# Kernel optimization log

Hardware: AMD Instinct MI355X
Metric: run time of the kernel (lower is better)

## Reference

```python
import jax, jax.numpy as jnp
import numpy as np

B, N, D, H = 8, 2048, 512, 512


def setup_inputs() -> dict:
    key = jax.random.key(0)
    kx, kwq, kbq, kwk, kbk = jax.random.split(key, 5)
    s = 1.0 / np.sqrt(D)
    return {
        "x": jax.random.normal(kx, (B, N, D), dtype=jnp.float32),
        "Wq": jax.random.uniform(kwq, (D, H), jnp.float32, -s, s),
        "bq": jax.random.uniform(kbq, (H,), jnp.float32, -s, s),
        "Wk": jax.random.uniform(kwk, (D, H), jnp.float32, -s, s),
        "bk": jax.random.uniform(kbk, (H,), jnp.float32, -s, s),
    }


def reference(x, Wq, bq, Wk, bk):
    # x: [B, N, D]
    q = jnp.einsum("bnd,dh->bnh", x, Wq) + bq          # [B, N, H]
    k = jnp.einsum("bnd,dh->bnh", x, Wk) + bk          # [B, N, H]
    energy = jnp.einsum("bih,bjh->bij", q, k)           # [B, N, N] (no scaling)
    # NOTE: softmax over dim=1 (the QUERY axis), not the usual key axis.
    attn = jax.nn.softmax(energy, axis=1)               # [B, N, N]
    out = jnp.einsum("bij,bjd->bid", attn, x)           # V = x
    return out
```

## Files before the change

### kernel.cpp

```cpp
#include <hip/hip_runtime.h>
#include <hip/hip_bf16.h>
#include <cstdio>

typedef float f32x4 __attribute__((ext_vector_type(4)));
typedef __bf16 bf16x8 __attribute__((ext_vector_type(8)));

static constexpr int Bn = 8, Nn = 2048, Dn = 512, Hn = 512;

__device__ __forceinline__ unsigned short f2bf(float x) {
    union { float f; unsigned int u; } v; v.f = x;
    unsigned int r = (v.u + 0x7FFFu + ((v.u >> 16) & 1u)) >> 16;
    return (unsigned short)r;
}
__device__ __forceinline__ float bf2f(unsigned short h) {
    union { unsigned int u; float f; } v; v.u = ((unsigned int)h) << 16;
    return v.f;
}

__device__ __forceinline__ void gload_lds16(const unsigned short* g, unsigned short* l) {
    __builtin_amdgcn_global_load_lds(
        (const __attribute__((address_space(1))) void*)g,
        (__attribute__((address_space(3))) void*)l,
        16, 0, 0);
}

__device__ __forceinline__ int xcd_swizzle(int lin, int nwg) {
    return (lin & 7) * (nwg >> 3) + (lin >> 3);
}

__global__ void cast_x_kernel(const float* __restrict__ x, unsigned short* __restrict__ xb, int n) {
    int i = (blockIdx.x * blockDim.x + threadIdx.x) * 8;
    if (i >= n) return;
    float4 a = *(const float4*)(x + i);
    float4 b = *(const float4*)(x + i + 4);
    unsigned short tmp[8] = {f2bf(a.x), f2bf(a.y), f2bf(a.z), f2bf(a.w),
                             f2bf(b.x), f2bf(b.y), f2bf(b.z), f2bf(b.w)};
    *(uint4*)(xb + i) = *(const uint4*)tmp;
}

__global__ __launch_bounds__(256) void transpose_cast_kernel(
    const float* __restrict__ in, unsigned short* __restrict__ out,
    const float* __restrict__ sdiv, int R, int C)
{
    __shared__ float tile[64][65];
    const int z = blockIdx.z;
    const float* inb = in + (size_t)z * R * C;
    unsigned short* outb = out + (size_t)z * R * C;
    const int r0 = blockIdx.y * 64, c0 = blockIdx.x * 64;
    const int tx = threadIdx.x & 63, ty = threadIdx.x >> 6;
#pragma unroll
    for (int p = 0; p < 64; p += 4) {
        const int r = p + ty;
        float v = inb[(size_t)(r0 + r) * C + c0 + tx];
        if (sdiv) v /= sdiv[(size_t)z * R + r0 + r];
        tile[r][tx] = v;
    }
    __syncthreads();
#pragma unroll
    for (int p = 0; p < 64; p += 4) {
        const int oc = p + ty;
        outb[(size_t)(c0 + oc) * R + r0 + tx] = f2bf(tile[tx][oc]);
    }
}

__global__ void combine_s_kernel(const float* __restrict__ s_part, float* __restrict__ s,
                                 int nblk, int total) {
    int i = blockIdx.x * blockDim.x + threadIdx.x;
    if (i >= total) return;
    int z = i >> 11, j = i & (Nn - 1);
    float acc = 0.f;
    for (int p = 0; p < nblk; ++p) acc += s_part[((size_t)z * nblk + p) * Nn + j];
    s[i] = acc;
}

template<int MODE>
__global__ __launch_bounds__(512, 2) void gemm8p(
    const unsigned short* __restrict__ A, long long sA, int lda,
    const unsigned short* __restrict__ Bt, long long sB, int ldb,
    void* __restrict__ Cp, long long sC,
    const float* __restrict__ bias, const float* __restrict__ bias2, int bsplit,
    float* __restrict__ s_part,
    int M, int N, int K, int gx, int gy)
{
    __shared__ unsigned short As[4][8192];
    __shared__ unsigned short Bs[4][8192];

    const int lin = xcd_swizzle(blockIdx.x, gridDim.x);
    const int bz = lin / (gx * gy);
    const int rem = lin - bz * gx * gy;
    const int by = rem / gx;
    const int bx = rem - by * gx;

    const unsigned short* Ab = A + (size_t)bz * sA;
    const unsigned short* Bb = Bt + (size_t)bz * sB;
    const int i0 = by * 256, j0 = bx * 256;

    const int t = threadIdx.x;
    const int lane = t & 63;
    const int w = t >> 6;
    const int wm = w >> 2, wn = w & 3;
    const int l15 = lane & 15, g = lane >> 4;

    const int rd_off = (l15 * 4 + (g ^ ((l15 >> 1) & 3))) * 16;
    const int grow = lane >> 2;
    const int gk = ((lane & 3) ^ ((lane >> 3) & 3)) * 8;

    f32x4 acc[8][4];
    const f32x4 zero4 = {0.f, 0.f, 0.f, 0.f};
#pragma unroll
    for (int mi = 0; mi < 8; ++mi)
#pragma unroll
        for (int nf = 0; nf < 4; ++nf) acc[mi][nf] = zero4;

    const int NT = K >> 6;

#define STAGE(baseP, ldP, r0P, ldsP, Tn, kh)                                             \
    {                                                                                    \
        const int _slot = ((Tn) & 1) * 2 + (kh);                                         \
        const unsigned short* _src = (baseP) + (size_t)((r0P) + w * 16 + grow) * (ldP)   \
                                     + (Tn) * 64 + (kh) * 32 + gk;                       \
        gload_lds16(_src, &ldsP[_slot][w * 512]);                                        \
        gload_lds16(_src + (size_t)128 * (ldP), &ldsP[_slot][(w + 8) * 512]);            \
    }

    STAGE(Ab, lda, i0, As, 0, 0);
    STAGE(Bb, ldb, j0, Bs, 0, 0);
    STAGE(Ab, lda, i0, As, 0, 1);
    STAGE(Bb, ldb, j0, Bs, 0, 1);

    bf16x8 bfv[4];

    for (int T = 0; T < NT; ++T) {
        const int sbase = (T & 1) * 2;
        const bool last = (T == NT - 1);
#pragma unroll
        for (int q = 0; q < 4; ++q) {
            const int kk = q >> 1, mh = q & 1;
            if (q == 0) {
                asm volatile("s_waitcnt vmcnt(4)" ::: "memory");
                asm volatile("s_barrier" ::: "memory");
            } else if (q == 2) {
                if (last) asm volatile("s_waitcnt vmcnt(0)" ::: "memory");
                else      asm volatile("s_waitcnt vmcnt(4)" ::: "memory");
                asm volatile("s_barrier" ::: "memory");
            }
            const char* Bbase = (const char*)&Bs[sbase + kk][0] + (wn * 4) * 1024 + rd_off;
            if (mh == 0) {
#pragma unroll
                for (int nf = 0; nf < 4; ++nf)
                    bfv[nf] = *(const bf16x8*)(Bbase + nf * 1024);
            }
            const char* Abase = (const char*)&As[sbase + kk][0] + (wm * 8 + mh * 4) * 1024 + rd_off;
            bf16x8 af[4];
#pragma unroll
            for (int mf = 0; mf < 4; ++mf)
                af[mf] = *(const bf16x8*)(Abase + mf * 1024);
            if (!last) {
                if (q == 0)      STAGE(Ab, lda, i0, As, T + 1, 0)
                else if (q == 1) STAGE(Bb, ldb, j0, Bs, T + 1, 0)
                else if (q == 2) STAGE(Ab, lda, i0, As, T + 1, 1)
                else             STAGE(Bb, ldb, j0, Bs, T + 1, 1)
            }
            __builtin_amdgcn_s_setprio(1);
#pragma unroll
            for (int mf = 0; mf < 4; ++mf)
#pragma unroll
                for (int nf = 0; nf < 4; ++nf)
                    acc[mh * 4 + mf][nf] =
                        __builtin_amdgcn_mfma_f32_16x16x32_bf16(af[mf], bfv[nf], acc[mh * 4 + mf][nf], 0, 0, 0);
            __builtin_amdgcn_s_setprio(0);
            asm volatile("s_barrier" ::: "memory");
        }
    }
#undef STAGE

    if (MODE == 0) {
        unsigned short* C = (unsigned short*)Cp;
#pragma unroll
        for (int nf = 0; nf < 4; ++nf) {
            const int col = j0 + wn * 64 + nf * 16 + l15;
            const float bv = (col < bsplit) ? bias[col] : bias2[col - bsplit];
#pragma unroll
            for (int mi = 0; mi < 8; ++mi) {
                const int rb = i0 + wm * 128 + (mi >> 2) * 64 + (mi & 3) * 16 + g * 4;
#pragma unroll
                for (int r = 0; r < 4; ++r)
                    C[(size_t)(rb + r) * N + col] = f2bf(acc[mi][nf][r] + bv);
            }
        }
    } else {
        unsigned short* C = (unsigned short*)Cp + (size_t)bz * sC;
        float cs[4] = {0.f, 0.f, 0.f, 0.f};
#pragma unroll
        for (int nf = 0; nf < 4; ++nf) {
            const int col = j0 + wn * 64 + nf * 16 + l15;
#pragma unroll
            for (int mi = 0; mi < 8; ++mi) {
                const int rb = i0 + wm * 128 + (mi >> 2) * 64 + (mi & 3) * 16 + g * 4;
#pragma unroll
                for (int r = 0; r < 4; ++r) {
                    const float e = __expf(acc[mi][nf][r]);
                    const unsigned short h = f2bf(e);
                    C[(size_t)(rb + r) * N + col] = h;
                    cs[nf] += bf2f(h);
                }
            }
        }
#pragma unroll
        for (int nf = 0; nf < 4; ++nf) {
            cs[nf] += __shfl_xor(cs[nf], 16);
            cs[nf] += __shfl_xor(cs[nf], 32);
        }
        __syncthreads();
        float* red = (float*)&As[0][0];
        if (g == 0) {
#pragma unroll
            for (int nf = 0; nf < 4; ++nf)
                red[wm * 256 + wn * 64 + nf * 16 + l15] = cs[nf];
        }
        __syncthreads();
        if (t < 256)
            s_part[((size_t)bz * gy + by) * Nn + j0 + t] = red[t] + red[256 + t];
    }
}

template<int MODE>
__global__ __launch_bounds__(256, 2) void gemm_bt(
    const unsigned short* __restrict__ A, long long sA, int lda,
    const unsigned short* __restrict__ Bt, long long sB, int ldb,
    void* __restrict__ Cp, long long sC,
    int M, int N, int K, int gx, int gy)
{
    __shared__ unsigned short As[128 * 64];
    __shared__ unsigned short Bs[128 * 64];

    const int lin = xcd_swizzle(blockIdx.x, gridDim.x);
    const int bz = lin / (gx * gy);
    const int rem = lin - bz * gx * gy;
    const int by = rem / gx;
    const int bx = rem - by * gx;

    const unsigned short* Ab = A + (size_t)bz * sA;
    const unsigned short* Bb = Bt + (size_t)bz * sB;
    const int i0 = by * 128, j0 = bx * 128;

    const int t = threadIdx.x;
    const int lane = t & 63;
    const int wave = t >> 6;
    const int wr = wave >> 1, wc = wave & 1;
    const int l15 = lane & 15, g = lane >> 4;

    f32x4 acc[4][4];
    const f32x4 zero4 = {0.f, 0.f, 0.f, 0.f};
#pragma unroll
    for (int mi = 0; mi < 4; ++mi)
#pragma unroll
        for (int ni = 0; ni < 4; ++ni) acc[mi][ni] = zero4;

    const int rbase = wave * 32;
    const int lrow = lane >> 3;
    const int gch = (lane & 7) ^ lrow;

    for (int kt = 0; kt < K; kt += 64) {
#pragma unroll
        for (int i = 0; i < 4; ++i) {
            const int r = rbase + i * 8 + lrow;
            gload_lds16(Ab + (size_t)(i0 + r) * lda + kt + gch * 8, As + (rbase + i * 8) * 64);
            gload_lds16(Bb + (size_t)(j0 + r) * ldb + kt + gch * 8, Bs + (rbase + i * 8) * 64);
        }
        __syncthreads();
#pragma unroll
        for (int kk = 0; kk < 64; kk += 32) {
            const int sl0 = (kk >> 3) + g;
            bf16x8 af[4], bfr[4];
#pragma unroll
            for (int mi = 0; mi < 4; ++mi) {
                const int row = wr * 64 + mi * 16 + l15;
                af[mi] = *(const bf16x8*)(As + row * 64 + ((sl0 ^ (row & 7)) * 8));
            }
#pragma unroll
            for (int ni = 0; ni < 4; ++ni) {
                const int row = wc * 64 + ni * 16 + l15;
                bfr[ni] = *(const bf16x8*)(Bs + row * 64 + ((sl0 ^ (row & 7)) * 8));
            }
#pragma unroll
            for (int mi = 0; mi < 4; ++mi)
#pragma unroll
                for (int ni = 0; ni < 4; ++ni)
                    acc[mi][ni] = __builtin_amdgcn_mfma_f32_16x16x32_bf16(af[mi], bfr[ni], acc[mi][ni], 0, 0, 0);
        }
        __syncthreads();
    }

    float* C = (float*)Cp + (size_t)bz * sC;
#pragma unroll
    for (int ni = 0; ni < 4; ++ni) {
        const int col = j0 + wc * 64 + ni * 16 + l15;
#pragma unroll
        for (int mi = 0; mi < 4; ++mi) {
            const int rb = i0 + wr * 64 + mi * 16 + g * 4;
#pragma unroll
            for (int r = 0; r < 4; ++r)
                C[(size_t)(rb + r) * N + col] = acc[mi][ni][r];
        }
    }
}

extern "C" void kernel_launch(void* const* d_in, const int* in_sizes, int n_in,
                              void* d_out, int out_size, void* d_ws, size_t ws_size,
                              hipStream_t stream) {
    const float* x  = (const float*)d_in[0];
    const float* Wq = (const float*)d_in[1];
    const float* bq = (const float*)d_in[2];
    const float* Wk = (const float*)d_in[3];
    const float* bk = (const float*)d_in[4];
    float* out = (float*)d_out;

    char* ws = (char*)d_ws;
    unsigned short* xb    = (unsigned short*)(ws);
    unsigned short* qk    = (unsigned short*)(ws + (16ull << 20));
    unsigned short* WqkT  = (unsigned short*)(ws + (48ull << 20));
    unsigned short* xsT   = (unsigned short*)(ws + (49ull << 20));
    float*          s_prt = (float*)(ws + (65ull << 20));
    float*          s     = (float*)(ws + (66ull << 20));
    unsigned short* expE  = (unsigned short*)(ws + (67ull << 20));
    if (ws_size < (131ull << 20)) {
        fprintf(stderr, "WS TOO SMALL: have %zu need %llu\n", ws_size, (131ull << 20));
    }

    cast_x_kernel<<<dim3((Bn * Nn * Dn) / (8 * 256)), 256, 0, stream>>>(x, xb, Bn * Nn * Dn);
    transpose_cast_kernel<<<dim3(Hn / 64, Dn / 64, 1), 256, 0, stream>>>(Wq, WqkT, nullptr, Dn, Hn);
    transpose_cast_kernel<<<dim3(Hn / 64, Dn / 64, 1), 256, 0, stream>>>(Wk, WqkT + (size_t)Hn * Dn, nullptr, Dn, Hn);
    {
        const int gx = (2 * Hn) / 256, gy = (Bn * Nn) / 256;
        gemm8p<0><<<dim3(gx * gy), 512, 0, stream>>>(
            xb, 0, Dn, WqkT, 0, Dn, qk, 0, bq, bk, Hn, nullptr,
            Bn * Nn, 2 * Hn, Dn, gx, gy);
    }
    {
        const int gx = Nn / 256, gy = Nn / 256;
        gemm8p<1><<<dim3(gx * gy * Bn), 512, 0, stream>>>(
            qk, (long long)Nn * 2 * Hn, 2 * Hn,
            qk + Hn, (long long)Nn * 2 * Hn, 2 * Hn,
            expE, (long long)Nn * Nn, nullptr, nullptr, 0, s_prt,
            Nn, Nn, Hn, gx, gy);
    }
    combine_s_kernel<<<dim3((Bn * Nn) / 256), 256, 0, stream>>>(s_prt, s, Nn / 256, Bn * Nn);
    transpose_cast_kernel<<<dim3(Dn / 64, Nn / 64, Bn), 256, 0, stream>>>(x, xsT, s, Nn, Dn);
    {
        const int gx = Dn / 128, gy = Nn / 128;
        gemm_bt<2><<<dim3(gx * gy * Bn), 256, 0, stream>>>(
            expE, (long long)Nn * Nn, Nn, xsT, (long long)Dn * Nn, Nn,
            out, (long long)Nn * Dn, Nn, Dn, Nn, gx, gy);
    }
}
```

Measured before the change: 156.8 us.

## Double-buffer PV GEMM LDS and restructure gemm8p inner loop barriers

```diff
diff --git a/kernel.cpp b/kernel.cpp
--- a/kernel.cpp
+++ b/kernel.cpp
@@ -128,80 +128,110 @@
     STAGE(Ab, lda, i0, As, 0, 1);
     STAGE(Bb, ldb, j0, Bs, 0, 1);
 
-    bf16x8 bfv[4];
-
     for (int T = 0; T < NT; ++T) {
         const int sbase = (T & 1) * 2;
         const bool last = (T == NT - 1);
-#pragma unroll
-        for (int q = 0; q < 4; ++q) {
-            const int kk = q >> 1, mh = q & 1;
-            if (q == 0) {
-                asm volatile("s_waitcnt vmcnt(4)" ::: "memory");
-                asm volatile("s_barrier" ::: "memory");
-            } else if (q == 2) {
-                if (last) asm volatile("s_waitcnt vmcnt(0)" ::: "memory");
-                else      asm volatile("s_waitcnt vmcnt(4)" ::: "memory");
-                asm volatile("s_barrier" ::: "memory");
-            }
-            const char* Bbase = (const char*)&Bs[sbase + kk][0] + (wn * 4) * 1024 + rd_off;
-            if (mh == 0) {
+
+        asm volatile("s_waitcnt vmcnt(4)" ::: "memory");
+        asm volatile("s_barrier" ::: "memory");
+        {
+            const char* Bbase = (const char*)&Bs[sbase][0] + wn * 4096 + rd_off;
+            const char* Abase = (const char*)&As[sbase][0] + wm * 8192 + rd_off;
+            bf16x8 bfv[4], af[4];
+#pragma unroll
+            for (int nf = 0; nf < 4; ++nf) bfv[nf] = *(const bf16x8*)(Bbase + nf * 1024);
+#pragma unroll
+            for (int mf = 0; mf < 4; ++mf) af[mf] = *(const bf16x8*)(Abase + mf * 1024);
+            if (!last) STAGE(Ab, lda, i0, As, T + 1, 0);
+            __builtin_amdgcn_s_setprio(1);
+#pragma unroll
+            for (int mf = 0; mf < 4; ++mf)
 #pragma unroll
                 for (int nf = 0; nf < 4; ++nf)
-                    bfv[nf] = *(const bf16x8*)(Bbase + nf * 1024);
-            }
-            const char* Abase = (const char*)&As[sbase + kk][0] + (wm * 8 + mh * 4) * 1024 + rd_off;
-            bf16x8 af[4];
+                    acc[mf][nf] = __builtin_amdgcn_mfma_f32_16x16x32_bf16(af[mf], bfv[nf], acc[mf][nf], 0, 0, 0);
+            __builtin_amdgcn_s_setprio(0);
+            bf16x8 ag[4];
+#pragma unroll
+            for (int mf = 0; mf < 4; ++mf) ag[mf] = *(const bf16x8*)(Abase + 4096 + mf * 1024);
+            if (!last) STAGE(Bb, ldb, j0, Bs, T + 1, 0);
+            __builtin_amdgcn_s_setprio(1);
 #pragma unroll
             for (int mf = 0; mf < 4; ++mf)
-                af[mf] = *(const bf16x8*)(Abase + mf * 1024);
-            if (!last) {
-                if (q == 0)      STAGE(Ab, lda, i0, As, T + 1, 0)
-                else if (q == 1) STAGE(Bb, ldb, j0, Bs, T + 1, 0)
-                else if (q == 2) STAGE(Ab, lda, i0, As, T + 1, 1)
-                else             STAGE(Bb, ldb, j0, Bs, T + 1, 1)
-            }
+#pragma unroll
+                for (int nf = 0; nf < 4; ++nf)
+                    acc[4 + mf][nf] = __builtin_amdgcn_mfma_f32_16x16x32_bf16(ag[mf], bfv[nf], acc[4 + mf][nf], 0, 0, 0);
+            __builtin_amdgcn_s_setprio(0);
+        }
+
+        if (last) asm volatile("s_waitcnt vmcnt(0)" ::: "memory");
+        else      asm volatile("s_waitcnt vmcnt(4)" ::: "memory");
+        asm volatile("s_barrier" ::: "memory");
+        {
+            const char* Bbase = (const char*)&Bs[sbase + 1][0] + wn * 4096 + rd_off;
+            const char* Abase = (const char*)&As[sbase + 1][0] + wm * 8192 + rd_off;
+            bf16x8 bfv[4], af[4];
+#pragma unroll
+            for (int nf = 0; nf < 4; ++nf) bfv[nf] = *(const bf16x8*)(Bbase + nf * 1024);
+#pragma unroll
+            for (int mf = 0; mf < 4; ++mf) af[mf] = *(const bf16x8*)(Abase + mf * 1024);
+            if (!last) STAGE(Ab, lda, i0, As, T + 1, 1);
             __builtin_amdgcn_s_setprio(1);
 #pragma unroll
             for (int mf = 0; mf < 4; ++mf)
 #pragma unroll
                 for (int nf = 0; nf < 4; ++nf)
-                    acc[mh * 4 + mf][nf] =
-                        __builtin_amdgcn_mfma_f32_16x16x32_bf16(af[mf], bfv[nf], acc[mh * 4 + mf][nf], 0, 0, 0);
+                    acc[mf][nf] = __builtin_amdgcn_mfma_f32_16x16x32_bf16(af[mf], bfv[nf], acc[mf][nf], 0, 0, 0);
             __builtin_amdgcn_s_setprio(0);
-            asm volatile("s_barrier" ::: "memory");
+            bf16x8 ag[4];
+#pragma unroll
+            for (int mf = 0; mf < 4; ++mf) ag[mf] = *(const bf16x8*)(Abase + 4096 + mf * 1024);
+            if (!last) STAGE(Bb, ldb, j0, Bs, T + 1, 1);
+            __builtin_amdgcn_s_setprio(1);
+#pragma unroll
+            for (int mf = 0; mf < 4; ++mf)
+#pragma unroll
+                for (int nf = 0; nf < 4; ++nf)
+                    acc[4 + mf][nf] = __builtin_amdgcn_mfma_f32_16x16x32_bf16(ag[mf], bfv[nf], acc[4 + mf][nf], 0, 0, 0);
+            __builtin_amdgcn_s_setprio(0);
         }
     }
 #undef STAGE
 
     if (MODE == 0) {
         unsigned short* C = (unsigned short*)Cp;
+        float bv[4];
 #pragma unroll
         for (int nf = 0; nf < 4; ++nf) {
             const int col = j0 + wn * 64 + nf * 16 + l15;
-            const float bv = (col < bsplit) ? bias[col] : bias2[col - bsplit];
-#pragma unroll
-            for (int mi = 0; mi < 8; ++mi) {
-                const int rb = i0 + wm * 128 + (mi >> 2) * 64 + (mi & 3) * 16 + g * 4;
-#pragma unroll
-                for (int r = 0; r < 4; ++r)
-                    C[(size_t)(rb + r) * N + col] = f2bf(acc[mi][nf][r] + bv);
+            bv[nf] = (col < bsplit) ? bias[col] : bias2[col - bsplit];
+        }
+        const int col0 = j0 + wn * 64 + l15;
+#pragma unroll
+        for (int mi = 0; mi < 8; ++mi) {
+            const int rb = i0 + wm * 128 + (mi >> 2) * 64 + (mi & 3) * 16 + g * 4;
+#pragma unroll
+            for (int r = 0; r < 4; ++r) {
+                unsigned short* Crow = C + (size_t)(rb + r) * N + col0;
+#pragma unroll
+                for (int nf = 0; nf < 4; ++nf)
+                    Crow[nf * 16] = f2bf(acc[mi][nf][r] + bv[nf]);
             }
         }
     } else {
         unsigned short* C = (unsigned short*)Cp + (size_t)bz * sC;
         float cs[4] = {0.f, 0.f, 0.f, 0.f};
-#pragma unroll
-        for (int nf = 0; nf < 4; ++nf) {
-            const int col = j0 + wn * 64 + nf * 16 + l15;
-#pragma unroll
-            for (int mi = 0; mi < 8; ++mi) {
-                const int rb = i0 + wm * 128 + (mi >> 2) * 64 + (mi & 3) * 16 + g * 4;
-#pragma unroll
-                for (int r = 0; r < 4; ++r) {
+        const int col0 = j0 + wn * 64 + l15;
+#pragma unroll
+        for (int mi = 0; mi < 8; ++mi) {
+            const int rb = i0 + wm * 128 + (mi >> 2) * 64 + (mi & 3) * 16 + g * 4;
+#pragma unroll
+            for (int r = 0; r < 4; ++r) {
+                unsigned short* Crow = C + (size_t)(rb + r) * N + col0;
+#pragma unroll
+                for (int nf = 0; nf < 4; ++nf) {
                     const float e = __expf(acc[mi][nf][r]);
                     const unsigned short h = f2bf(e);
-                    C[(size_t)(rb + r) * N + col] = h;
+                    Crow[nf * 16] = h;
                     cs[nf] += bf2f(h);
                 }
             }
@@ -224,15 +254,14 @@
     }
 }
 
-template<int MODE>
-__global__ __launch_bounds__(256, 2) void gemm_bt(
+__global__ __launch_bounds__(256, 2) void gemm_pv(
     const unsigned short* __restrict__ A, long long sA, int lda,
     const unsigned short* __restrict__ Bt, long long sB, int ldb,
-    void* __restrict__ Cp, long long sC,
+    float* __restrict__ Cp, long long sC,
     int M, int N, int K, int gx, int gy)
 {
-    __shared__ unsigned short As[128 * 64];
-    __shared__ unsigned short Bs[128 * 64];
+    __shared__ unsigned short As[2][128 * 64];
+    __shared__ unsigned short Bs[2][128 * 64];
 
     const int lin = xcd_swizzle(blockIdx.x, gridDim.x);
     const int bz = lin / (gx * gy);
@@ -261,14 +290,26 @@
     const int lrow = lane >> 3;
     const int gch = (lane & 7) ^ lrow;
 
-    for (int kt = 0; kt < K; kt += 64) {
-#pragma unroll
-        for (int i = 0; i < 4; ++i) {
-            const int r = rbase + i * 8 + lrow;
-            gload_lds16(Ab + (size_t)(i0 + r) * lda + kt + gch * 8, As + (rbase + i * 8) * 64);
-            gload_lds16(Bb + (size_t)(j0 + r) * ldb + kt + gch * 8, Bs + (rbase + i * 8) * 64);
-        }
-        __syncthreads();
+#define STAGEPV(s, ktv)                                                        \
+    {                                                                          \
+        _Pragma("unroll")                                                      \
+        for (int i = 0; i < 4; ++i) {                                          \
+            const int r = rbase + i * 8 + lrow;                                \
+            gload_lds16(Ab + (size_t)(i0 + r) * lda + (ktv) + gch * 8,         \
+                        &As[s][(rbase + i * 8) * 64]);                         \
+            gload_lds16(Bb + (size_t)(j0 + r) * ldb + (ktv) + gch * 8,         \
+                        &Bs[s][(rbase + i * 8) * 64]);                         \
+        }                                                                      \
+    }
+
+    STAGEPV(0, 0);
+    asm volatile("s_waitcnt vmcnt(0)" ::: "memory");
+    asm volatile("s_barrier" ::: "memory");
+
+    const int NT = K >> 6;
+    for (int T = 0; T < NT; ++T) {
+        const int cur = T & 1;
+        if (T + 1 < NT) STAGEPV(cur ^ 1, (T + 1) * 64);
 #pragma unroll
         for (int kk = 0; kk < 64; kk += 32) {
             const int sl0 = (kk >> 3) + g;
@@ -276,23 +317,27 @@
 #pragma unroll
             for (int mi = 0; mi < 4; ++mi) {
                 const int row = wr * 64 + mi * 16 + l15;
-                af[mi] = *(const bf16x8*)(As + row * 64 + ((sl0 ^ (row & 7)) * 8));
+                af[mi] = *(const bf16x8*)(&As[cur][0] + row * 64 + ((sl0 ^ (row & 7)) * 8));
             }
 #pragma unroll
             for (int ni = 0; ni < 4; ++ni) {
                 const int row = wc * 64 + ni * 16 + l15;
-                bfr[ni] = *(const bf16x8*)(Bs + row * 64 + ((sl0 ^ (row & 7)) * 8));
+                bfr[ni] = *(const bf16x8*)(&Bs[cur][0] + row * 64 + ((sl0 ^ (row & 7)) * 8));
             }
+            __builtin_amdgcn_s_setprio(1);
 #pragma unroll
             for (int mi = 0; mi < 4; ++mi)
 #pragma unroll
                 for (int ni = 0; ni < 4; ++ni)
                     acc[mi][ni] = __builtin_amdgcn_mfma_f32_16x16x32_bf16(af[mi], bfr[ni], acc[mi][ni], 0, 0, 0);
-        }
-        __syncthreads();
-    }
-
-    float* C = (float*)Cp + (size_t)bz * sC;
+            __builtin_amdgcn_s_setprio(0);
+        }
+        asm volatile("s_waitcnt vmcnt(0)" ::: "memory");
+        asm volatile("s_barrier" ::: "memory");
+    }
+#undef STAGEPV
+
+    float* C = Cp + (size_t)bz * sC;
 #pragma unroll
     for (int ni = 0; ni < 4; ++ni) {
         const int col = j0 + wc * 64 + ni * 16 + l15;
@@ -349,7 +394,7 @@
     transpose_cast_kernel<<<dim3(Dn / 64, Nn / 64, Bn), 256, 0, stream>>>(x, xsT, s, Nn, Dn);
     {
         const int gx = Dn / 128, gy = Nn / 128;
-        gemm_bt<2><<<dim3(gx * gy * Bn), 256, 0, stream>>>(
+        gemm_pv<<<dim3(gx * gy * Bn), 256, 0, stream>>>(
             expE, (long long)Nn * Nn, Nn, xsT, (long long)Dn * Nn, Nn,
             out, (long long)Nn * Dn, Nn, Dn, Nn, gx, gy);
     }
```

Measured after the change: 144.2 us. 1.09x faster.
